# Optimization experiments

Hardware: AMD Instinct MI355X
Metric: run time of the kernel (lower is better)

## Reference

```python
import jax, jax.numpy as jnp
import numpy as np

EMB = 512
GP = 128
NH = 8
HD = EMB // NH  # 64
B = 2
S = 1024


def _rel_shift(x):
    # Faithful port of DoubleAttentionLayer._rel_shift (pads dim 1, reinterprets
    # (B, J+1, K, n) as (J+1, B, K, n), drops first slice). Row-major reshape
    # semantics match torch .view on contiguous tensors exactly.
    Bsz, J, K, N = x.shape
    zp = jnp.zeros((Bsz, 1, K, N), x.dtype)
    xp = jnp.concatenate([zp, x], axis=1).reshape(J + 1, Bsz, K, N)
    return xp[1:].reshape(Bsz, J, K, N)


def _layernorm(x):
    # nn.LayerNorm(emb_dim, elementwise_affine=False), eps=1e-5
    m = jnp.mean(x, axis=-1, keepdims=True)
    v = jnp.var(x, axis=-1, keepdims=True)
    return (x - m) / jnp.sqrt(v + 1e-5)


def _attention(q, k, v, Bc, Bp, gpe, mask, Wp_w, Wp_b):
    Bsz, J, E = q.shape
    K = k.shape[1]
    # content scores
    qc = jnp.tanh((q + Bc).reshape(Bsz, J, NH, HD))
    kh = jnp.tanh(k.reshape(Bsz, K, NH, HD))
    ctx = jnp.einsum('bjnd,bknd->bjkn', qc, kh)
    # position scores (tanh before reshape in source for qp -- elementwise, same math)
    qp = jnp.tanh(q + Bp).reshape(Bsz, J, NH, HD)
    kp = jnp.tanh((gpe @ Wp_w + Wp_b).reshape(Bsz, -1, NH, HD))
    pos = jnp.einsum('bjnd,bknd->bjkn', qp, kp)
    pad = ctx.shape[2] - pos.shape[2]  # static; 0 in this configuration
    if pad > 0:
        # replicate-pad pos at front of k dim; constant(0)-pad mask (torch F.pad defaults)
        pos = jnp.concatenate([jnp.broadcast_to(pos[:, :, :1], (Bsz, J, pad, NH)), pos], axis=2)
        mask = jnp.concatenate([jnp.zeros(mask.shape[:2] + (pad, mask.shape[3]), mask.dtype), mask], axis=2)
    pos = _rel_shift(pos)
    att = (ctx + pos) / (HD ** 0.5) - 1e30 * mask
    att = jax.nn.softmax(att, axis=2)
    vh = jnp.tanh(v.reshape(Bsz, K, NH, HD))
    return jnp.einsum('bjkn,bknd->bjnd', att, vh).reshape(Bsz, J, E)


def setup_inputs() -> dict:
    key = jax.random.key(0)
    ks = jax.random.split(key, 12)
    u_emb = jax.random.normal(ks[0], (B, S, EMB), jnp.float32)
    f_emb = jax.random.normal(ks[1], (B, S, EMB), jnp.float32)
    gpe = jax.random.normal(ks[2], (B, S, GP), jnp.float32)
    # causal masks: 1 where attention is disallowed, broadcast over heads
    causal = (1.0 - jnp.tril(jnp.ones((S, S), jnp.float32)))[None, :, :, None]
    u_mask = jnp.broadcast_to(causal, (B, S, S, 1))
    f_mask = jnp.broadcast_to(causal, (B, S, S, 1))
    w = 0.02
    Wq_w = w * jax.random.normal(ks[3], (EMB, EMB), jnp.float32)
    Wq_b = jnp.zeros((EMB,), jnp.float32)
    Wkv_w = w * jax.random.normal(ks[4], (EMB, 2 * EMB), jnp.float32)
    Wkv_b = jnp.zeros((2 * EMB,), jnp.float32)
    Wp_w = w * jax.random.normal(ks[5], (GP, EMB), jnp.float32)
    Wp_b = jnp.zeros((EMB,), jnp.float32)
    Wu_w = w * jax.random.normal(ks[6], (EMB, EMB), jnp.float32)
    Wu_b = jnp.zeros((EMB,), jnp.float32)
    Bfc = 0.2 * jax.random.normal(ks[7], (1, 1, EMB), jnp.float32)
    Bfp = 0.2 * jax.random.normal(ks[8], (1, 1, EMB), jnp.float32)
    Buc = 0.2 * jax.random.normal(ks[9], (1, 1, EMB), jnp.float32)
    Bup = 0.2 * jax.random.normal(ks[10], (1, 1, EMB), jnp.float32)
    return {"u_emb": u_emb, "f_emb": f_emb, "gpe": gpe, "u_mask": u_mask, "f_mask": f_mask,
            "Wq_w": Wq_w, "Wq_b": Wq_b, "Wkv_w": Wkv_w, "Wkv_b": Wkv_b,
            "Wp_w": Wp_w, "Wp_b": Wp_b, "Wu_w": Wu_w, "Wu_b": Wu_b,
            "Bfc": Bfc, "Bfp": Bfp, "Buc": Buc, "Bup": Bup}


def reference(u_emb, f_emb, gpe, u_mask, f_mask, Wq_w, Wq_b, Wkv_w, Wkv_b,
              Wp_w, Wp_b, Wu_w, Wu_b, Bfc, Bfp, Buc, Bup):
    # first_part=True path: f_mem = f_emb (memory buffer registration has no output effect)
    q_u = f_emb @ Wu_w + Wu_b
    kv = f_emb @ Wkv_w + Wkv_b
    k, v = jnp.split(kv, 2, axis=-1)
    u_out = _layernorm(u_emb + _attention(q_u, k, v, Buc, Bup, gpe, u_mask, Wp_w, Wp_b))
    # last_layer=False: second attention over f stream
    q_f = f_emb @ Wq_w + Wq_b
    f_out = _layernorm(f_emb + _attention(q_f, k, v, Bfc, Bfp, gpe, f_mask, Wp_w, Wp_b))
    return (u_out, f_out)
```

## Files before the change

kernel.cpp:

```cpp
#include <hip/hip_runtime.h>
#include <math.h>

#define EMB 512
#define NH 8
#define HD 64
#define BB 2
#define SS 1024
#define ROWS (BB * SS)

typedef __attribute__((ext_vector_type(8))) short bhalf8;
typedef __attribute__((ext_vector_type(4))) float f32x4;
typedef __attribute__((ext_vector_type(8))) unsigned short us8;
typedef unsigned short ushort_t;

typedef const __attribute__((address_space(1))) void gas_void;
typedef __attribute__((address_space(3))) void las_void;

__device__ __forceinline__ void gl2lds16(const void* g, void* l) {
  __builtin_amdgcn_global_load_lds((gas_void*)g, (las_void*)l, 16, 0, 0);
}

__device__ __forceinline__ unsigned short f2bf(float x) {
  unsigned u = __float_as_uint(x);
  u = (u + 0x7FFFu + ((u >> 16) & 1u)) >> 16;
  return (unsigned short)u;
}
__device__ __forceinline__ float bf2f(unsigned short v) {
  return __uint_as_float(((unsigned)v) << 16);
}
__device__ __forceinline__ float fast_tanh(float x) {
  x = fminf(15.f, fmaxf(-15.f, x));
  const float e = __expf(2.f * x);
  return (e - 1.f) / (e + 1.f);
}

__global__ __launch_bounds__(256) void prep_kernel(
    const float* __restrict__ f_emb, const float* __restrict__ gpe,
    const float* __restrict__ Wu, const float* __restrict__ Wq,
    const float* __restrict__ Wkv, const float* __restrict__ Wp,
    ushort_t* __restrict__ fembB, ushort_t* __restrict__ gpeB,
    ushort_t* __restrict__ WuT, ushort_t* __restrict__ WqT,
    ushort_t* __restrict__ WkvT, ushort_t* __restrict__ WpT,
    ushort_t* __restrict__ Qcomb) {
  __shared__ __align__(16) ushort_t sT[64 * 72];
  const int bid = blockIdx.x;
  const int tid = threadIdx.x;

  if (bid < 160) {
    const bool isF = bid < 128;
    const float* src = isF ? f_emb : gpe;
    ushort_t* dst = isF ? fembB : gpeB;
    const size_t base = (size_t)(isF ? bid : bid - 128) * 8192;
#pragma unroll
    for (int j = 0; j < 4; ++j) {
      const size_t off = base + ((size_t)j * 256 + tid) * 8;
      const float4 a = *(const float4*)&src[off];
      const float4 b = *(const float4*)&src[off + 4];
      us8 o;
      o[0] = f2bf(a.x); o[1] = f2bf(a.y); o[2] = f2bf(a.z); o[3] = f2bf(a.w);
      o[4] = f2bf(b.x); o[5] = f2bf(b.y); o[6] = f2bf(b.z); o[7] = f2bf(b.w);
      *(us8*)&dst[off] = o;
    }
  } else if (bid < 432) {
    int t = bid - 160;
    const float* W;
    ushort_t* WT;
    int Nw, Kd, k0, n0;
    if (t < 64) {
      W = Wu; WT = WuT; Nw = 512; Kd = 512;
      k0 = (t >> 3) * 64; n0 = (t & 7) * 64;
    } else if (t < 128) {
      t -= 64; W = Wq; WT = WqT; Nw = 512; Kd = 512;
      k0 = (t >> 3) * 64; n0 = (t & 7) * 64;
    } else if (t < 256) {
      t -= 128; W = Wkv; WT = WkvT; Nw = 1024; Kd = 512;
      k0 = (t >> 4) * 64; n0 = (t & 15) * 64;
    } else {
      t -= 256; W = Wp; WT = WpT; Nw = 512; Kd = 128;
      k0 = (t >> 3) * 64; n0 = (t & 7) * 64;
    }
    const int kk = tid >> 2, seg = tid & 3;
    const float* src = &W[(size_t)(k0 + kk) * Nw + n0 + seg * 16];
    float v[16];
    *(float4*)&v[0] = *(const float4*)&src[0];
    *(float4*)&v[4] = *(const float4*)&src[4];
    *(float4*)&v[8] = *(const float4*)&src[8];
    *(float4*)&v[12] = *(const float4*)&src[12];
#pragma unroll
    for (int i = 0; i < 16; ++i) sT[(seg * 16 + i) * 72 + kk] = f2bf(v[i]);
    __syncthreads();
#pragma unroll
    for (int p = 0; p < 2; ++p) {
      const int idx = p * 256 + tid;
      const int n = idx >> 3, c8 = (idx & 7) * 8;
      const us8 o = *(const us8*)&sT[n * 72 + c8];
      *(us8*)&WT[(size_t)(n0 + n) * Kd + k0 + c8] = o;
    }
  } else {
    const int t2 = tid >> 7, rem = tid & 127;
    const int h = rem >> 4, d4 = (rem & 15) * 4;
    *(ushort4*)&Qcomb[((size_t)t2 * ROWS + 1023) * 1024 + h * 128 + 64 + d4] =
        make_ushort4(0, 0, 0, 0);
  }
}

__global__ __launch_bounds__(256, 3) void projpe_kernel(
    const ushort_t* __restrict__ fembB, const ushort_t* __restrict__ gpeB,
    const ushort_t* __restrict__ WuT, const ushort_t* __restrict__ WqT,
    const ushort_t* __restrict__ WkvT, const ushort_t* __restrict__ WpT,
    const float* __restrict__ Wu_b, const float* __restrict__ Wq_b,
    const float* __restrict__ Wkv_b, const float* __restrict__ Wp_b,
    const float* __restrict__ Buc, const float* __restrict__ Bup,
    const float* __restrict__ Bfc, const float* __restrict__ Bfp,
    ushort_t* __restrict__ Qcomb, ushort_t* __restrict__ Kcomb,
    ushort_t* __restrict__ vhT) {
  const int bx = blockIdx.x;
  const int mb = blockIdx.y * 128;
  const int tid = threadIdx.x;
  const int w = tid >> 6, lane = tid & 63;
  const int ln = lane & 15, quad = lane >> 4;
  const int wm = (w >> 1) * 64, wn = (w & 1) * 32;

  __shared__ __align__(16) ushort_t sMem[24576];

  const bool isPe = (bx >= 32);
  const int nb = isPe ? 0 : bx * 64;
  const int npbase = isPe ? (bx - 32) * 64 : 0;
  const ushort_t* Asrc = isPe ? gpeB : fembB;
  const int lda = isPe ? 128 : 512;
  const int trips = isPe ? 2 : 8;

  const ushort_t* Wt;
  int Kd, coff;
  if (isPe) { Wt = WpT; Kd = 128; coff = npbase; }
  else if (nb < 512) { Wt = WuT; Kd = 512; coff = nb; }
  else if (nb < 1024) { Wt = WqT; Kd = 512; coff = nb - 512; }
  else { Wt = WkvT; Kd = 512; coff = nb - 1024; }

  const int l3 = lane >> 3, c7 = lane & 7;
  const int swz = (c7 ^ l3) * 8;

#define STAGE_PP(T_, P_)                                                     \
  {                                                                          \
    const int k1_ = (T_) * 64;                                               \
    ushort_t* dA_ = sMem + (P_) * 8192;                                      \
    ushort_t* dB_ = sMem + 16384 + (P_) * 4096;                              \
    _Pragma("unroll") for (int s_ = 0; s_ < 4; ++s_) {                       \
      const int q_ = w * 4 + s_;                                             \
      const int r_ = q_ * 8 + l3;                                            \
      gl2lds16(&Asrc[(size_t)(mb + r_) * lda + k1_ + swz], &dA_[q_ * 512]);  \
    }                                                                        \
    _Pragma("unroll") for (int s_ = 0; s_ < 2; ++s_) {                       \
      const int q_ = w * 2 + s_;                                             \
      const int r_ = q_ * 8 + l3;                                            \
      gl2lds16(&Wt[(size_t)(coff + r_) * Kd + k1_ + swz], &dB_[q_ * 512]);   \
    }                                                                        \
  }

  f32x4 acc[4][2];
#pragma unroll
  for (int rt = 0; rt < 4; ++rt)
#pragma unroll
    for (int ct = 0; ct < 2; ++ct) acc[rt][ct] = (f32x4){0.f, 0.f, 0.f, 0.f};

  STAGE_PP(0, 0);

  for (int t0 = 0; t0 < trips; ++t0) {
    __syncthreads();
    if (t0 < trips - 1) STAGE_PP(t0 + 1, (t0 + 1) & 1);
    const ushort_t* bA = sMem + (t0 & 1) * 8192;
    const ushort_t* bB = sMem + 16384 + (t0 & 1) * 4096;
#pragma unroll
    for (int kc = 0; kc < 2; ++kc) {
      bhalf8 af[4], bfr[2];
#pragma unroll
      for (int rt = 0; rt < 4; ++rt) {
        const int row = wm + rt * 16 + ln;
        af[rt] = *(const bhalf8*)&bA[row * 64 +
                                     (((kc * 4 + quad) ^ (row & 7)) << 3)];
      }
#pragma unroll
      for (int ct = 0; ct < 2; ++ct) {
        const int row = wn + ct * 16 + ln;
        bfr[ct] = *(const bhalf8*)&bB[row * 64 +
                                      (((kc * 4 + quad) ^ (row & 7)) << 3)];
      }
#pragma unroll
      for (int rt = 0; rt < 4; ++rt)
#pragma unroll
        for (int ct = 0; ct < 2; ++ct)
          acc[rt][ct] = __builtin_amdgcn_mfma_f32_16x16x32_bf16(
              af[rt], bfr[ct], acc[rt][ct], 0, 0, 0);
    }
  }

  __syncthreads();
  ushort_t* sOut = sMem;

  if (!isPe && nb >= 1536) {
#pragma unroll
    for (int ct = 0; ct < 2; ++ct) {
      const int nl = wn + ct * 16 + ln;
      const float wb = Wkv_b[nb + nl - 1024];
#pragma unroll
      for (int rt = 0; rt < 4; ++rt)
#pragma unroll
        for (int r = 0; r < 4; ++r) {
          const int ml = wm + rt * 16 + quad * 4 + r;
          sOut[nl * 136 + ml] = f2bf(fast_tanh(acc[rt][ct][r] + wb));
        }
    }
    __syncthreads();
    const int b = mb >> 10, mo = mb & 1023;
#pragma unroll
    for (int i = 0; i < 4; ++i) {
      const int idx = tid + i * 256;
      const int nl = idx >> 4, m8 = (idx & 15) * 8;
      const us8 v = *(const us8*)&sOut[nl * 136 + m8];
      *(us8*)&vhT[((size_t)b * 512 + (nb - 1536) + nl) * 1024 + mo + m8] = v;
    }
  } else {
    const float* WB =
        isPe ? Wp_b : (nb < 512 ? Wu_b : (nb < 1024 ? Wq_b : Wkv_b));
    const int woff =
        isPe ? npbase : (nb < 512 ? nb : (nb < 1024 ? nb - 512 : nb - 1024));
    const bool rawDump = (!isPe && nb < 1024);
#pragma unroll
    for (int ct = 0; ct < 2; ++ct) {
      const int nl = wn + ct * 16 + ln;
      const float wb = WB[woff + nl];
#pragma unroll
      for (int rt = 0; rt < 4; ++rt)
#pragma unroll
        for (int r = 0; r < 4; ++r) {
          const int ml = wm + rt * 16 + quad * 4 + r;
          const float v = acc[rt][ct][r] + wb;
          sOut[ml * 72 + nl] = f2bf(rawDump ? v : fast_tanh(v));
        }
    }
    __syncthreads();
#pragma unroll
    for (int i = 0; i < 4; ++i) {
      const int idx = tid + i * 256;
      const int rr = idx >> 3, c8 = (idx & 7) * 8;
      const int m = mb + rr;
      const us8 v = *(const us8*)&sOut[rr * 72 + c8];
      if (isPe) {
        const int n = npbase + c8;
        const int h = n >> 6;
        *(us8*)&Kcomb[(size_t)m * 1024 + h * 128 + 64 + (n & 63)] = v;
      } else if (nb < 1024) {
        const int strm = nb >= 512 ? 1 : 0;
        const int n = (nb - strm * 512) + c8;
        const int h = n >> 6;
        const float* BC = strm ? Bfc : Buc;
        const float* BP = strm ? Bfp : Bup;
        float bcA[8], bpA[8];
        *(float4*)&bcA[0] = *(const float4*)&BC[n];
        *(float4*)&bcA[4] = *(const float4*)&BC[n + 4];
        *(float4*)&bpA[0] = *(const float4*)&BP[n];
        *(float4*)&bpA[4] = *(const float4*)&BP[n + 4];
        us8 oc, op;
#pragma unroll
        for (int jj = 0; jj < 8; ++jj) {
          const float vv = bf2f((unsigned short)v[jj]);
          oc[jj] = f2bf(fast_tanh(vv + bcA[jj]));
          op[jj] = f2bf(fast_tanh(vv + bpA[jj]));
        }
        *(us8*)&Qcomb[((size_t)strm * ROWS + m) * 1024 + h * 128 + (n & 63)] =
            oc;
        if (m != 0) {
          const int mp = (m < 1024) ? m - 1 : m;
          *(us8*)&Qcomb[((size_t)strm * ROWS + mp) * 1024 + h * 128 + 64 +
                        (n & 63)] = op;
        }
      } else {
        const int n = (nb - 1024) + c8;
        const int h = n >> 6;
        *(us8*)&Kcomb[(size_t)m * 1024 + h * 128 + (n & 63)] = v;
      }
    }
  }
}

__global__ __launch_bounds__(256, 2) void attn_kernel(
    const ushort_t* __restrict__ Qcomb, const ushort_t* __restrict__ Kcomb,
    const ushort_t* __restrict__ vhT, float* __restrict__ Ofin) {
  const int pbid = blockIdx.x;
  const int lbid = (pbid & 7) * 64 + (pbid >> 3);
  const int c = lbid >> 4, jt = lbid & 15;
  const int tid = threadIdx.x;
  const int w = tid >> 6, lane = tid & 63;
  const int ln = lane & 15, quad = lane >> 4;
  const int l4 = lane >> 4, p15 = lane & 15;
  const int l3 = lane >> 3, l7 = lane & 7;
  const int t = c >> 4, b = (c >> 3) & 1, h = c & 7;

  __shared__ __align__(16) ushort_t sK[2 * 8192];
  __shared__ __align__(16) ushort_t sV[2 * 4096];
  __shared__ __align__(16) ushort_t sP[64 * 72];

#define STAGE_KV(KT_, BUF_)                                                   \
  {                                                                           \
    const size_t kb_ = ((size_t)b * SS + (KT_)*64) * 1024 + h * 128;          \
    ushort_t* bk_ = sK + (BUF_)*8192;                                         \
    _Pragma("unroll") for (int s_ = 0; s_ < 4; ++s_) {                        \
      const int q_ = w * 4 + s_;                                              \
      const int r_ = q_ * 4 + l4;                                             \
      const int gl_ = p15 ^ (r_ & 7);                                         \
      gl2lds16(&Kcomb[kb_ + (size_t)r_ * 1024 + gl_ * 8], &bk_[q_ * 512]);    \
    }                                                                         \
    const size_t vb_ = ((size_t)b * 512 + h * 64) * 1024 + (KT_)*64;          \
    ushort_t* bv_ = sV + (BUF_)*4096;                                         \
    _Pragma("unroll") for (int s_ = 0; s_ < 2; ++s_) {                        \
      const int q_ = w * 2 + s_;                                              \
      const int r_ = q_ * 8 + l3;                                             \
      const int gl_ = l7 ^ (r_ & 7);                                          \
      gl2lds16(&vhT[vb_ + (size_t)r_ * 1024 + gl_ * 8], &bv_[q_ * 512]);      \
    }                                                                         \
  }

  STAGE_KV(0, 0);

  bhalf8 aq[4];
  {
    const size_t qb_ =
        ((size_t)t * ROWS + b * SS + jt * 64 + w * 16 + ln) * 1024 + h * 128 +
        quad * 8;
#pragma unroll
    for (int kc = 0; kc < 4; ++kc)
      aq[kc] = *(const bhalf8*)&Qcomb[qb_ + kc * 32];
  }

  f32x4 oacc[4];
#pragma unroll
  for (int ct = 0; ct < 4; ++ct) oacc[ct] = (f32x4){0.f, 0.f, 0.f, 0.f};
  float lsum[4] = {0.f, 0.f, 0.f, 0.f};

  for (int kt = 0; kt <= jt; ++kt) {
    __syncthreads();
    const ushort_t* bK = sK + (kt & 1) * 8192;
    const ushort_t* bV = sV + (kt & 1) * 4096;
    if (kt < jt) STAGE_KV(kt + 1, (kt + 1) & 1);

    f32x4 sacc[4];
#pragma unroll
    for (int ct = 0; ct < 4; ++ct) {
      sacc[ct] = (f32x4){0.f, 0.f, 0.f, 0.f};
#pragma unroll
      for (int kc = 0; kc < 4; ++kc) {
        const bhalf8 bk = *(const bhalf8*)&bK[(ct * 16 + ln) * 128 +
                                              (((kc * 4 + quad) ^ l7) << 3)];
        sacc[ct] = __builtin_amdgcn_mfma_f32_16x16x32_bf16(aq[kc], bk,
                                                           sacc[ct], 0, 0, 0);
      }
    }

    const bool diag = (kt == jt);
#pragma unroll
    for (int ct = 0; ct < 4; ++ct)
#pragma unroll
      for (int r = 0; r < 4; ++r) {
        float p;
        if (diag && (ct * 16 + ln > w * 16 + quad * 4 + r))
          p = 0.f;
        else
          p = __expf(sacc[ct][r] * 0.125f - 16.f);
        sacc[ct][r] = p;
        lsum[r] += p;
      }

#pragma unroll
    for (int ct = 0; ct < 4; ++ct)
#pragma unroll
      for (int r = 0; r < 4; ++r)
        sP[(w * 16 + quad * 4 + r) * 72 + ct * 16 + ln] =
            (ushort_t)(__float_as_uint(sacc[ct][r]) >> 16);

    asm volatile("s_waitcnt lgkmcnt(0)" ::: "memory");
    __builtin_amdgcn_sched_barrier(0);

#pragma unroll
    for (int kc = 0; kc < 2; ++kc) {
      const bhalf8 ap =
          *(const bhalf8*)&sP[(w * 16 + ln) * 72 + kc * 32 + quad * 8];
#pragma unroll
      for (int ct = 0; ct < 4; ++ct) {
        const bhalf8 bv = *(const bhalf8*)&bV[(ct * 16 + ln) * 64 +
                                              (((kc * 4 + quad) ^ l7) << 3)];
        oacc[ct] = __builtin_amdgcn_mfma_f32_16x16x32_bf16(ap, bv, oacc[ct],
                                                           0, 0, 0);
      }
    }
  }

#pragma unroll
  for (int r = 0; r < 4; ++r) {
    float s = lsum[r];
    s += __shfl_xor(s, 1);
    s += __shfl_xor(s, 2);
    s += __shfl_xor(s, 4);
    s += __shfl_xor(s, 8);
    const float rinv = 1.f / s;
    const int j = jt * 64 + w * 16 + quad * 4 + r;
    const size_t orow = (((size_t)t * ROWS + b * SS + j) << 9) + h * 64;
#pragma unroll
    for (int ct = 0; ct < 4; ++ct)
      Ofin[orow + ct * 16 + ln] = oacc[ct][r] * rinv;
  }
}

__global__ __launch_bounds__(256) void ln_kernel(
    const float* __restrict__ u_emb, const float* __restrict__ f_emb,
    const float* __restrict__ Ofin, float* __restrict__ out) {
  const int rid = blockIdx.x * 4 + (threadIdx.x >> 6);
  const int lane = threadIdx.x & 63;
  const int t = rid >> 11, row = rid & 2047;
  const float* resid = t ? f_emb : u_emb;
  const size_t base = (size_t)row * 512;
  const size_t obase = ((size_t)t * ROWS + row) * 512;
  const int o = lane * 8;

  const float4 n0 = *(const float4*)&Ofin[obase + o];
  const float4 n1 = *(const float4*)&Ofin[obase + o + 4];
  const float4 r0 = *(const float4*)&resid[base + o];
  const float4 r1 = *(const float4*)&resid[base + o + 4];
  float y[8];
  y[0] = r0.x + n0.x; y[1] = r0.y + n0.y;
  y[2] = r0.z + n0.z; y[3] = r0.w + n0.w;
  y[4] = r1.x + n1.x; y[5] = r1.y + n1.y;
  y[6] = r1.z + n1.z; y[7] = r1.w + n1.w;

  float s = 0.f, q = 0.f;
#pragma unroll
  for (int i = 0; i < 8; ++i) {
    s += y[i];
    q += y[i] * y[i];
  }
#pragma unroll
  for (int off = 1; off < 64; off <<= 1) {
    s += __shfl_xor(s, off);
    q += __shfl_xor(q, off);
  }
  const float mean = s * (1.f / 512.f);
  const float var = q * (1.f / 512.f) - mean * mean;
  const float rstd = rsqrtf(var + 1e-5f);

  float4 o0, o1;
  o0.x = (y[0] - mean) * rstd; o0.y = (y[1] - mean) * rstd;
  o0.z = (y[2] - mean) * rstd; o0.w = (y[3] - mean) * rstd;
  o1.x = (y[4] - mean) * rstd; o1.y = (y[5] - mean) * rstd;
  o1.z = (y[6] - mean) * rstd; o1.w = (y[7] - mean) * rstd;
  *(float4*)&out[obase + o] = o0;
  *(float4*)&out[obase + o + 4] = o1;
}

extern "C" void kernel_launch(void* const* d_in, const int* in_sizes, int n_in,
                              void* d_out, int out_size, void* d_ws,
                              size_t ws_size, hipStream_t stream) {
  (void)in_sizes; (void)n_in; (void)out_size; (void)ws_size;
  const float* u_emb = (const float*)d_in[0];
  const float* f_emb = (const float*)d_in[1];
  const float* gpe = (const float*)d_in[2];
  const float* Wq_w = (const float*)d_in[5];
  const float* Wq_b = (const float*)d_in[6];
  const float* Wkv_w = (const float*)d_in[7];
  const float* Wkv_b = (const float*)d_in[8];
  const float* Wp_w = (const float*)d_in[9];
  const float* Wp_b = (const float*)d_in[10];
  const float* Wu_w = (const float*)d_in[11];
  const float* Wu_b = (const float*)d_in[12];
  const float* Bfc = (const float*)d_in[13];
  const float* Bfp = (const float*)d_in[14];
  const float* Buc = (const float*)d_in[15];
  const float* Bup = (const float*)d_in[16];
  float* out = (float*)d_out;

  ushort_t* ws = (ushort_t*)d_ws;
  const size_t SZ = (size_t)ROWS * EMB;
  ushort_t* Qcomb = ws;
  ushort_t* Kcomb = ws + 4 * SZ;
  ushort_t* vhT = ws + 6 * SZ;
  float* Ofin = (float*)(ws + 7 * SZ);
  ushort_t* fembB = ws + 12 * SZ;
  ushort_t* gpeB = ws + 13 * SZ;
  ushort_t* WuT = ws + 13 * SZ + SZ / 4;
  ushort_t* WqT = ws + 13 * SZ + SZ / 2;
  ushort_t* WkvT = ws + 13 * SZ + 3 * (SZ / 4);
  ushort_t* WpT = ws + 13 * SZ + 5 * (SZ / 4);

  dim3 blk(256);
  hipLaunchKernelGGL(prep_kernel, dim3(433), blk, 0, stream, f_emb, gpe, Wu_w,
                     Wq_w, Wkv_w, Wp_w, fembB, gpeB, WuT, WqT, WkvT, WpT,
                     Qcomb);
  hipLaunchKernelGGL(projpe_kernel, dim3(40, 16), blk, 0, stream, fembB, gpeB,
                     WuT, WqT, WkvT, WpT, Wu_b, Wq_b, Wkv_b, Wp_b, Buc, Bup,
                     Bfc, Bfp, Qcomb, Kcomb, vhT);
  hipLaunchKernelGGL(attn_kernel, dim3(512), blk, 0, stream, Qcomb, Kcomb,
                     vhT, Ofin);
  hipLaunchKernelGGL(ln_kernel, dim3(1024), blk, 0, stream, u_emb, f_emb,
                     Ofin, out);
}
```

Before: 146.7 us.

## Use 128-row query tiles in attention and store attention output as bf16

Each attention block now handles 128 query rows instead of 64, so every staged K/V tile is reused across two 16-row MFMA subtiles per wave, and the grid is halved to 256 blocks. The causal mask becomes a per-element row/column comparison that runs on every tile. The attention output buffer changes from fp32 to bf16 and the layernorm kernel reads it as bf16, which halves that intermediate's traffic but lowers its precision. The risks are higher register pressure from doubled accumulators, load imbalance from fewer and more uneven blocks, and extra masking and exp work on the half-masked diagonal tiles.

```diff
diff --git a/kernel.cpp b/kernel.cpp
--- a/kernel.cpp
+++ b/kernel.cpp
@@ -285,10 +285,10 @@
 
 __global__ __launch_bounds__(256, 2) void attn_kernel(
     const ushort_t* __restrict__ Qcomb, const ushort_t* __restrict__ Kcomb,
-    const ushort_t* __restrict__ vhT, float* __restrict__ Ofin) {
+    const ushort_t* __restrict__ vhT, ushort_t* __restrict__ Ofin) {
   const int pbid = blockIdx.x;
-  const int lbid = (pbid & 7) * 64 + (pbid >> 3);
-  const int c = lbid >> 4, jt = lbid & 15;
+  const int lbid = (pbid & 7) * 32 + (pbid >> 3);
+  const int c = lbid >> 3, J = lbid & 7;
   const int tid = threadIdx.x;
   const int w = tid >> 6, lane = tid & 63;
   const int ln = lane & 15, quad = lane >> 4;
@@ -298,7 +298,7 @@
 
   __shared__ __align__(16) ushort_t sK[2 * 8192];
   __shared__ __align__(16) ushort_t sV[2 * 4096];
-  __shared__ __align__(16) ushort_t sP[64 * 72];
+  __shared__ __align__(16) ushort_t sP[128 * 72];
 
 #define STAGE_KV(KT_, BUF_)                                                   \
   {                                                                           \
@@ -322,97 +322,123 @@
 
   STAGE_KV(0, 0);
 
-  bhalf8 aq[4];
-  {
+  bhalf8 aq[2][4];
+#pragma unroll
+  for (int rt = 0; rt < 2; ++rt) {
     const size_t qb_ =
-        ((size_t)t * ROWS + b * SS + jt * 64 + w * 16 + ln) * 1024 + h * 128 +
-        quad * 8;
+        ((size_t)t * ROWS + b * SS + J * 128 + w * 32 + rt * 16 + ln) * 1024 +
+        h * 128 + quad * 8;
 #pragma unroll
     for (int kc = 0; kc < 4; ++kc)
-      aq[kc] = *(const bhalf8*)&Qcomb[qb_ + kc * 32];
-  }
-
-  f32x4 oacc[4];
-#pragma unroll
-  for (int ct = 0; ct < 4; ++ct) oacc[ct] = (f32x4){0.f, 0.f, 0.f, 0.f};
-  float lsum[4] = {0.f, 0.f, 0.f, 0.f};
-
-  for (int kt = 0; kt <= jt; ++kt) {
+      aq[rt][kc] = *(const bhalf8*)&Qcomb[qb_ + kc * 32];
+  }
+
+  f32x4 oacc[2][4];
+#pragma unroll
+  for (int rt = 0; rt < 2; ++rt)
+#pragma unroll
+    for (int ct = 0; ct < 4; ++ct) oacc[rt][ct] = (f32x4){0.f, 0.f, 0.f, 0.f};
+  float lsum[2][4];
+#pragma unroll
+  for (int rt = 0; rt < 2; ++rt)
+#pragma unroll
+    for (int r = 0; r < 4; ++r) lsum[rt][r] = 0.f;
+
+  const int NT = 2 * J + 2;
+  for (int kt = 0; kt < NT; ++kt) {
     __syncthreads();
     const ushort_t* bK = sK + (kt & 1) * 8192;
     const ushort_t* bV = sV + (kt & 1) * 4096;
-    if (kt < jt) STAGE_KV(kt + 1, (kt + 1) & 1);
-
-    f32x4 sacc[4];
-#pragma unroll
-    for (int ct = 0; ct < 4; ++ct) {
-      sacc[ct] = (f32x4){0.f, 0.f, 0.f, 0.f};
-#pragma unroll
-      for (int kc = 0; kc < 4; ++kc) {
+    if (kt < NT - 1) STAGE_KV(kt + 1, (kt + 1) & 1);
+
+    f32x4 sacc[2][4];
+#pragma unroll
+    for (int rt = 0; rt < 2; ++rt)
+#pragma unroll
+      for (int ct = 0; ct < 4; ++ct)
+        sacc[rt][ct] = (f32x4){0.f, 0.f, 0.f, 0.f};
+#pragma unroll
+    for (int kc = 0; kc < 4; ++kc) {
+#pragma unroll
+      for (int ct = 0; ct < 4; ++ct) {
         const bhalf8 bk = *(const bhalf8*)&bK[(ct * 16 + ln) * 128 +
                                               (((kc * 4 + quad) ^ l7) << 3)];
-        sacc[ct] = __builtin_amdgcn_mfma_f32_16x16x32_bf16(aq[kc], bk,
-                                                           sacc[ct], 0, 0, 0);
+#pragma unroll
+        for (int rt = 0; rt < 2; ++rt)
+          sacc[rt][ct] = __builtin_amdgcn_mfma_f32_16x16x32_bf16(
+              aq[rt][kc], bk, sacc[rt][ct], 0, 0, 0);
       }
     }
 
-    const bool diag = (kt == jt);
-#pragma unroll
-    for (int ct = 0; ct < 4; ++ct)
-#pragma unroll
-      for (int r = 0; r < 4; ++r) {
-        float p;
-        if (diag && (ct * 16 + ln > w * 16 + quad * 4 + r))
-          p = 0.f;
-        else
-          p = __expf(sacc[ct][r] * 0.125f - 16.f);
-        sacc[ct][r] = p;
-        lsum[r] += p;
-      }
-
-#pragma unroll
-    for (int ct = 0; ct < 4; ++ct)
-#pragma unroll
-      for (int r = 0; r < 4; ++r)
-        sP[(w * 16 + quad * 4 + r) * 72 + ct * 16 + ln] =
-            (ushort_t)(__float_as_uint(sacc[ct][r]) >> 16);
+#pragma unroll
+    for (int rt = 0; rt < 2; ++rt)
+#pragma unroll
+      for (int ct = 0; ct < 4; ++ct)
+#pragma unroll
+        for (int r = 0; r < 4; ++r) {
+          const int qrow = J * 128 + w * 32 + rt * 16 + quad * 4 + r;
+          const int kcol = kt * 64 + ct * 16 + ln;
+          float p;
+          if (kcol > qrow)
+            p = 0.f;
+          else
+            p = __expf(sacc[rt][ct][r] * 0.125f - 16.f);
+          sacc[rt][ct][r] = p;
+          lsum[rt][r] += p;
+        }
+
+#pragma unroll
+    for (int rt = 0; rt < 2; ++rt)
+#pragma unroll
+      for (int ct = 0; ct < 4; ++ct)
+#pragma unroll
+        for (int r = 0; r < 4; ++r)
+          sP[(w * 32 + rt * 16 + quad * 4 + r) * 72 + ct * 16 + ln] =
+              (ushort_t)(__float_as_uint(sacc[rt][ct][r]) >> 16);
 
     asm volatile("s_waitcnt lgkmcnt(0)" ::: "memory");
     __builtin_amdgcn_sched_barrier(0);
 
 #pragma unroll
     for (int kc = 0; kc < 2; ++kc) {
-      const bhalf8 ap =
-          *(const bhalf8*)&sP[(w * 16 + ln) * 72 + kc * 32 + quad * 8];
+      bhalf8 ap[2];
+#pragma unroll
+      for (int rt = 0; rt < 2; ++rt)
+        ap[rt] = *(const bhalf8*)&sP[(w * 32 + rt * 16 + ln) * 72 + kc * 32 +
+                                     quad * 8];
 #pragma unroll
       for (int ct = 0; ct < 4; ++ct) {
         const bhalf8 bv = *(const bhalf8*)&bV[(ct * 16 + ln) * 64 +
                                               (((kc * 4 + quad) ^ l7) << 3)];
-        oacc[ct] = __builtin_amdgcn_mfma_f32_16x16x32_bf16(ap, bv, oacc[ct],
-                                                           0, 0, 0);
+#pragma unroll
+        for (int rt = 0; rt < 2; ++rt)
+          oacc[rt][ct] = __builtin_amdgcn_mfma_f32_16x16x32_bf16(
+              ap[rt], bv, oacc[rt][ct], 0, 0, 0);
       }
     }
   }
 
 #pragma unroll
-  for (int r = 0; r < 4; ++r) {
-    float s = lsum[r];
-    s += __shfl_xor(s, 1);
-    s += __shfl_xor(s, 2);
-    s += __shfl_xor(s, 4);
-    s += __shfl_xor(s, 8);
-    const float rinv = 1.f / s;
-    const int j = jt * 64 + w * 16 + quad * 4 + r;
-    const size_t orow = (((size_t)t * ROWS + b * SS + j) << 9) + h * 64;
-#pragma unroll
-    for (int ct = 0; ct < 4; ++ct)
-      Ofin[orow + ct * 16 + ln] = oacc[ct][r] * rinv;
-  }
+  for (int rt = 0; rt < 2; ++rt)
+#pragma unroll
+    for (int r = 0; r < 4; ++r) {
+      float s = lsum[rt][r];
+      s += __shfl_xor(s, 1);
+      s += __shfl_xor(s, 2);
+      s += __shfl_xor(s, 4);
+      s += __shfl_xor(s, 8);
+      const float rinv = 1.f / s;
+      const int j = J * 128 + w * 32 + rt * 16 + quad * 4 + r;
+      const size_t orow = (((size_t)t * ROWS + b * SS + j) << 9) + h * 64;
+#pragma unroll
+      for (int ct = 0; ct < 4; ++ct)
+        Ofin[orow + ct * 16 + ln] = f2bf(oacc[rt][ct][r] * rinv);
+    }
 }
 
 __global__ __launch_bounds__(256) void ln_kernel(
     const float* __restrict__ u_emb, const float* __restrict__ f_emb,
-    const float* __restrict__ Ofin, float* __restrict__ out) {
+    const ushort_t* __restrict__ Ofin, float* __restrict__ out) {
   const int rid = blockIdx.x * 4 + (threadIdx.x >> 6);
   const int lane = threadIdx.x & 63;
   const int t = rid >> 11, row = rid & 2047;
@@ -421,15 +447,14 @@
   const size_t obase = ((size_t)t * ROWS + row) * 512;
   const int o = lane * 8;
 
-  const float4 n0 = *(const float4*)&Ofin[obase + o];
-  const float4 n1 = *(const float4*)&Ofin[obase + o + 4];
+  const us8 nv = *(const us8*)&Ofin[obase + o];
   const float4 r0 = *(const float4*)&resid[base + o];
   const float4 r1 = *(const float4*)&resid[base + o + 4];
   float y[8];
-  y[0] = r0.x + n0.x; y[1] = r0.y + n0.y;
-  y[2] = r0.z + n0.z; y[3] = r0.w + n0.w;
-  y[4] = r1.x + n1.x; y[5] = r1.y + n1.y;
-  y[6] = r1.z + n1.z; y[7] = r1.w + n1.w;
+  y[0] = r0.x + bf2f(nv[0]); y[1] = r0.y + bf2f(nv[1]);
+  y[2] = r0.z + bf2f(nv[2]); y[3] = r0.w + bf2f(nv[3]);
+  y[4] = r1.x + bf2f(nv[4]); y[5] = r1.y + bf2f(nv[5]);
+  y[6] = r1.z + bf2f(nv[6]); y[7] = r1.w + bf2f(nv[7]);
 
   float s = 0.f, q = 0.f;
 #pragma unroll
@@ -481,7 +506,7 @@
   ushort_t* Qcomb = ws;
   ushort_t* Kcomb = ws + 4 * SZ;
   ushort_t* vhT = ws + 6 * SZ;
-  float* Ofin = (float*)(ws + 7 * SZ);
+  ushort_t* Ofin = ws + 7 * SZ;
   ushort_t* fembB = ws + 12 * SZ;
   ushort_t* gpeB = ws + 13 * SZ;
   ushort_t* WuT = ws + 13 * SZ + SZ / 4;
@@ -496,7 +521,7 @@
   hipLaunchKernelGGL(projpe_kernel, dim3(40, 16), blk, 0, stream, fembB, gpeB,
                      WuT, WqT, WkvT, WpT, Wu_b, Wq_b, Wkv_b, Wp_b, Buc, Bup,
                      Bfc, Bfp, Qcomb, Kcomb, vhT);
-  hipLaunchKernelGGL(attn_kernel, dim3(512), blk, 0, stream, Qcomb, Kcomb,
+  hipLaunchKernelGGL(attn_kernel, dim3(256), blk, 0, stream, Qcomb, Kcomb,
                      vhT, Ofin);
   hipLaunchKernelGGL(ln_kernel, dim3(1024), blk, 0, stream, u_emb, f_emb,
                      Ofin, out);
```

Result: slower. 149.9 us (+2.2%).
